# Optimization experiments

Measured on AMD Instinct MI355X. Metric: run time of the kernel, lower is better.

## Reference

```python
import jax, jax.numpy as jnp
import numpy as np

B, L = 16384, 200
N_USERS, N_ITEMS, N_CATS, N_DUR = 1_000_000, 100_000, 1000, 50
UD, ID, CD, DD, SD = 64, 64, 16, 8, 64
UDENSE, IDENSE = 25, 3
CONCAT = UD + ID + CD + DD + UDENSE + IDENSE + SD  # 244
NE, EH, EO, NT = 8, 256, 128, 2
T1, T2 = 64, 32  # tower dims
AH1, AH2 = 64, 16  # DIN attention hidden dims
NEG_INF = -1e9


def setup_inputs() -> dict:
    key = jax.random.key(0)
    ks = iter(jax.random.split(key, 40))
    nrm = lambda shape, s: jax.random.normal(next(ks), shape, jnp.float32) * s
    inp = {
        'user_id': jax.random.randint(next(ks), (B,), 0, N_USERS),
        'item_id': jax.random.randint(next(ks), (B,), 0, N_ITEMS),
        'item_category': jax.random.randint(next(ks), (B,), 0, N_CATS),
        'item_dur_bkt': jax.random.randint(next(ks), (B,), 0, N_DUR),
        'user_dense': jax.random.normal(next(ks), (B, UDENSE), jnp.float32),
        'item_dense': jax.random.normal(next(ks), (B, IDENSE), jnp.float32),
        'history_seq': jax.random.randint(next(ks), (B, L), 0, N_ITEMS + 1),
    }
    # embeddings (std=0.01 as in _init_weights); hist row 0 is padding_idx -> zero
    inp['user_E'] = nrm((N_USERS, UD), 0.01)
    inp['item_E'] = nrm((N_ITEMS, ID), 0.01)
    inp['cat_E'] = nrm((N_CATS, CD), 0.01)
    inp['dur_E'] = nrm((N_DUR, DD), 0.01)
    inp['hist_E'] = nrm((N_ITEMS + 1, SD), 0.01).at[0].set(0.0)
    inp['Wproj'] = nrm((ID, SD), 0.12)  # xavier-ish for target_proj (no bias)
    # DIN attention MLP: 4*SD -> 64 -> 16 -> 1
    inp['aW1'] = nrm((4 * SD, AH1), 0.06); inp['ab1'] = jnp.zeros((AH1,), jnp.float32)
    inp['aW2'] = nrm((AH1, AH2), 0.15);    inp['ab2'] = jnp.zeros((AH2,), jnp.float32)
    inp['aW3'] = nrm((AH2, 1), 0.3);       inp['ab3'] = jnp.zeros((1,), jnp.float32)
    # stacked experts: concat -> 256 -> 128 (ReLU both)
    inp['eW1'] = nrm((NE, CONCAT, EH), 0.06); inp['eb1'] = jnp.zeros((NE, EH), jnp.float32)
    inp['eW2'] = nrm((NE, EH, EO), 0.06);     inp['eb2'] = jnp.zeros((NE, EO), jnp.float32)
    # per-task gates: concat -> NE softmax
    inp['gW'] = nrm((NT, CONCAT, NE), 0.06); inp['gb'] = jnp.zeros((NT, NE), jnp.float32)
    # stacked towers: 128 -> 64 -> 32 -> 1
    inp['tW1'] = nrm((NT, EO, T1), 0.09); inp['tb1'] = jnp.zeros((NT, T1), jnp.float32)
    inp['tW2'] = nrm((NT, T1, T2), 0.12); inp['tb2'] = jnp.zeros((NT, T2), jnp.float32)
    inp['tW3'] = nrm((NT, T2, 1), 0.17);  inp['tb3'] = jnp.zeros((NT, 1), jnp.float32)
    return inp


def reference(user_id, item_id, item_category, item_dur_bkt, user_dense, item_dense,
              history_seq, user_E, item_E, cat_E, dur_E, hist_E, Wproj,
              aW1, ab1, aW2, ab2, aW3, ab3,
              eW1, eb1, eW2, eb2, gW, gb,
              tW1, tb1, tW2, tb2, tW3, tb3):
    # --- feature encoding ---
    i_emb = item_E[item_id]            # (B, ID)
    u_emb = user_E[user_id]            # (B, UD)
    c_emb = cat_E[item_category]       # (B, CD)
    d_emb = dur_E[item_dur_bkt]        # (B, DD)
    h_emb = hist_E[history_seq]        # (B, L, SD)
    tgt = (i_emb @ Wproj)[:, None, :]  # (B, 1, SD)
    t = jnp.broadcast_to(tgt, h_emb.shape)
    # DIN attention features: [target, hist, target-hist, target*hist]
    feat = jnp.concatenate([t, h_emb, t - h_emb, t * h_emb], axis=-1)  # (B, L, 4*SD)
    h = jax.nn.relu(feat @ aW1 + ab1)
    h = jax.nn.relu(h @ aW2 + ab2)
    scores = (h @ aW3 + ab3)[..., 0]   # (B, L)
    scores = jnp.where(history_seq == 0, NEG_INF, scores)
    attn = jax.nn.softmax(scores, axis=-1)
    pooled = jnp.einsum('bl,bld->bd', attn, h_emb)  # (B, SD)
    shared = jnp.concatenate([u_emb, i_emb, c_emb, d_emb, user_dense, item_dense, pooled], axis=-1)  # (B, CONCAT)
    # --- experts (batched GEMM) ---
    eh = jax.nn.relu(jnp.einsum('bc,ech->beh', shared, eW1) + eb1)
    eo = jax.nn.relu(jnp.einsum('beh,eho->beo', eh, eW2) + eb2)  # (B, NE, EO)
    # --- per-task gating + towers ---
    gate = jax.nn.softmax(jnp.einsum('bc,tce->bte', shared, gW) + gb, axis=-1)  # (B, T, NE)
    ti = jnp.einsum('bte,beo->bto', gate, eo)  # (B, T, EO)
    x = jax.nn.relu(jnp.einsum('bto,toh->bth', ti, tW1) + tb1)
    x = jax.nn.relu(jnp.einsum('bth,thk->btk', x, tW2) + tb2)
    logit = (jnp.einsum('btk,tkj->btj', x, tW3) + tb3)[..., 0]  # (B, T)
    pred = jax.nn.sigmoid(logit)
    return pred[:, 0], pred[:, 1]
```

## Files before the change

kernel.cpp:

```cpp
#include <hip/hip_runtime.h>
#include <hip/hip_bf16.h>
#include <cstdint>
#include <cmath>


typedef __attribute__((ext_vector_type(8))) short bfrag;
typedef __attribute__((ext_vector_type(4))) float f32x4;

__device__ __forceinline__ unsigned short f2bf(float f) {
  __hip_bfloat16 h = __float2bfloat16(f);
  return __builtin_bit_cast(unsigned short, h);
}
__device__ __forceinline__ float bf2f(unsigned short b) {
  union { unsigned u; float f; } v; v.u = ((unsigned)b) << 16;
  return v.f;
}
__device__ __forceinline__ float bfLo(unsigned hv) {
  union { unsigned u; float f; } v; v.u = hv << 16;
  return v.f;
}
__device__ __forceinline__ float bfHi(unsigned hv) {
  union { unsigned u; float f; } v; v.u = hv & 0xffff0000u;
  return v.f;
}

#define SWZ(row, col) ((col) ^ (((row) & 7) << 3))

static constexpr size_t WS_ATTNB = 0;
static constexpr size_t WS_AW2T  = WS_ATTNB + 16384;
static constexpr size_t WS_A13   = WS_AW2T + 2048;
static constexpr size_t WS_EW1T  = WS_A13 + 16384;
static constexpr size_t WS_EW2T  = WS_EW1T + 1048576;
static constexpr size_t WS_HISTB = WS_EW2T + 524288;
static constexpr size_t WS_TGT   = WS_HISTB + 12800256;
static constexpr size_t WS_TA    = WS_TGT + 2097152;
static constexpr size_t WS_SHP   = WS_TA + 4194304;
static constexpr size_t WS_EO    = WS_SHP + 8388608;
static constexpr size_t WS_GWB   = WS_EO + 33554432;
static constexpr size_t WS_TW1B  = WS_GWB + 8192;
static constexpr size_t WS_TW2B  = WS_TW1B + 32768;

__launch_bounds__(256)
__global__ void k0_prep(const float* __restrict__ aW1, const float* __restrict__ aW2,
                        const float* __restrict__ eW1, const float* __restrict__ eW2,
                        const float* __restrict__ hist_E,
                        const float* __restrict__ gW, const float* __restrict__ tW1,
                        const float* __restrict__ tW2,
                        unsigned short* __restrict__ attnBt, unsigned short* __restrict__ aW2t,
                        float* __restrict__ A13,
                        unsigned short* __restrict__ eW1t, unsigned short* __restrict__ eW2t,
                        unsigned short* __restrict__ hist_b,
                        unsigned short* __restrict__ gWb, unsigned short* __restrict__ tW1b,
                        unsigned short* __restrict__ tW2b) {
  int tid = blockIdx.x * blockDim.x + threadIdx.x;
  int nth = gridDim.x * blockDim.x;
  for (int i = tid; i < 64 * 128; i += nth) {
    int n = i >> 7, k = i & 127;
    float v = (k < 64) ? (aW1[(64 + k) * 64 + n] - aW1[(128 + k) * 64 + n])
                       : aW1[(128 + k) * 64 + n];
    attnBt[i] = f2bf(v);
  }
  for (int i = tid; i < 64 * 64; i += nth) {
    int k = i >> 6, n = i & 63;
    A13[i] = aW1[k * 64 + n] + aW1[(128 + k) * 64 + n];
  }
  for (int i = tid; i < 16 * 64; i += nth) {
    int n = i >> 6, k = i & 63;
    aW2t[i] = f2bf(aW2[k * 16 + n]);
  }
  for (int i = tid; i < 8 * 256 * 256; i += nth) {
    int e = i >> 16, n = (i >> 8) & 255, k = i & 255;
    eW1t[i] = (k < 244) ? f2bf(eW1[(e * 244 + k) * 256 + n]) : (unsigned short)0;
  }
  for (int i = tid; i < 8 * 128 * 256; i += nth) {
    int e = i >> 15, n = (i >> 8) & 127, k = i & 255;
    eW2t[i] = f2bf(eW2[(e * 256 + k) * 128 + n]);
  }
  for (int i = tid; i < 16 * 256; i += nth) {
    int n = i >> 8, k = i & 255, t = n >> 3, e = n & 7;
    gWb[i] = (k < 244) ? f2bf(gW[(t * 244 + k) * 8 + e]) : (unsigned short)0;
  }
  for (int i = tid; i < 2 * 64 * 128; i += nth) {
    int t = i >> 13, n = (i >> 7) & 63, k = i & 127;
    tW1b[i] = f2bf(tW1[(t * 128 + k) * 64 + n]);
  }
  for (int i = tid; i < 2 * 32 * 64; i += nth) {
    int t = i >> 11, n = (i >> 6) & 31, k = i & 63;
    tW2b[i] = f2bf(tW2[(t * 64 + k) * 32 + n]);
  }
  for (int i = tid; i < 100001 * 64; i += nth) hist_b[i] = f2bf(hist_E[i]);
}

__launch_bounds__(256)
__global__ void k1_tgt(const int* __restrict__ item_id, const float* __restrict__ item_E,
                       const float* __restrict__ Wproj, const float* __restrict__ A13,
                       const float* __restrict__ ab1,
                       unsigned short* __restrict__ tgt, float* __restrict__ tA) {
  __shared__ float Wp[64 * 64], A13s[64 * 64], ab1s[64];
  __shared__ float ivb[4][64], tbuf[4][64];
  int tid = threadIdx.x, w = tid >> 6, lane = tid & 63;
  for (int i = tid; i < 4096; i += 256) { Wp[i] = Wproj[i]; A13s[i] = A13[i]; }
  if (tid < 64) ab1s[tid] = ab1[tid];
  __syncthreads();
  int b0 = blockIdx.x * 16;
  for (int it = 0; it < 4; ++it) {
    int b = b0 + w * 4 + it;
    int iid = item_id[b];
    ivb[w][lane] = item_E[(size_t)iid * 64 + lane];
    __syncthreads();
    float t = 0.f;
#pragma unroll 8
    for (int k = 0; k < 64; ++k) t += ivb[w][k] * Wp[k * 64 + lane];
    tbuf[w][lane] = t;
    __syncthreads();
    float ta = ab1s[lane];
#pragma unroll 8
    for (int k = 0; k < 64; ++k) ta += tbuf[w][k] * A13s[k * 64 + lane];
    tgt[(size_t)b * 64 + lane] = f2bf(t);
    tA[(size_t)b * 64 + lane] = ta;
  }
}

__launch_bounds__(256)
__global__ void k3a_assemble(const int* __restrict__ user_id, const int* __restrict__ item_id,
                             const int* __restrict__ item_cat, const int* __restrict__ item_dur,
                             const float* __restrict__ user_dense, const float* __restrict__ item_dense,
                             const float* __restrict__ user_E, const float* __restrict__ item_E,
                             const float* __restrict__ cat_E, const float* __restrict__ dur_E,
                             unsigned short* __restrict__ shared_p) {
  int tid = threadIdx.x, w = tid >> 6, lane = tid & 63;
  int b = blockIdx.x * 4 + w;
  unsigned short* row = shared_p + (size_t)b * 256;
  row[lane]      = f2bf(user_E[(size_t)user_id[b] * 64 + lane]);
  row[64 + lane] = f2bf(item_E[(size_t)item_id[b] * 64 + lane]);
  if (lane < 16) row[128 + lane] = f2bf(cat_E[item_cat[b] * 16 + lane]);
  if (lane < 8)  row[144 + lane] = f2bf(dur_E[item_dur[b] * 8 + lane]);
  if (lane < 25) row[152 + lane] = f2bf(user_dense[b * 25 + lane]);
  if (lane < 3)  row[177 + lane] = f2bf(item_dense[b * 3 + lane]);
  if (lane < 12) row[244 + lane] = 0;
}

__launch_bounds__(256, 5)
__global__ void k2_attn(const int* __restrict__ hist_seq, const unsigned short* __restrict__ hist_b,
                        const unsigned short* __restrict__ tgt, const float* __restrict__ tA,
                        const unsigned short* __restrict__ attnBt_g, const unsigned short* __restrict__ aW2t_g,
                        const float* __restrict__ ab2, const float* __restrict__ aW3,
                        unsigned short* __restrict__ shared_p) {
  __shared__ unsigned short sH1[208 * 64];
  __shared__ int   ids[208];
  __shared__ float tv[64], tAv[64];
  __shared__ float sSc[208];
  __shared__ float red[8];
  __shared__ float pbuf[512];
  int b = blockIdx.x;
  int tid = threadIdx.x, w = tid >> 6, lane = tid & 63;
  int lr = lane & 15, g = lane >> 4;

  if (tid < 208) ids[tid] = (tid < 200) ? hist_seq[(size_t)b * 200 + tid] : 0;
  if (tid < 64) tv[tid] = bf2f(tgt[(size_t)b * 64 + tid]);
  else if (tid < 128) tAv[tid - 64] = tA[(size_t)b * 64 + (tid - 64)];

  bfrag b2fr[2];
#pragma unroll
  for (int kk = 0; kk < 2; ++kk)
    b2fr[kk] = *(const bfrag*)(aW2t_g + lr * 64 + kk * 32 + g * 8);
  float ab2v = ab2[lr];
  float aW3v = aW3[lr];
  __syncthreads();

  {
    int n = tid >> 2, k0 = (tid & 3) * 16;
    const unsigned short* rowp = attnBt_g + n * 128;
    unsigned short a23[16], a4[16], mo[16];
    *(uint4*)(a23)     = *(const uint4*)(rowp + k0);
    *(uint4*)(a23 + 8) = *(const uint4*)(rowp + k0 + 8);
    *(uint4*)(a4)      = *(const uint4*)(rowp + 64 + k0);
    *(uint4*)(a4 + 8)  = *(const uint4*)(rowp + 64 + k0 + 8);
#pragma unroll
    for (int i = 0; i < 16; ++i)
      mo[i] = f2bf(bf2f(a23[i]) + tv[k0 + i] * bf2f(a4[i]));
    *(uint4*)(sH1 + n * 64 + SWZ(n, k0))     = *(uint4*)(mo);
    *(uint4*)(sH1 + n * 64 + SWZ(n, k0 + 8)) = *(uint4*)(mo + 8);
  }
  __syncthreads();
  bfrag bfr[4][2];
#pragma unroll
  for (int nt = 0; nt < 4; ++nt)
#pragma unroll
    for (int kk = 0; kk < 2; ++kk) {
      int n = nt * 16 + lr;
      bfr[nt][kk] = *(const bfrag*)(sH1 + n * 64 + SWZ(n, kk * 32 + g * 8));
    }
  __syncthreads();

  for (int mt = w; mt < 13; mt += 4) {
    int m = mt * 16 + lr;
    const unsigned short* hrow = hist_b + (size_t)ids[m] * 64;
    bfrag h0 = *(const bfrag*)(hrow + g * 8);
    bfrag h1 = *(const bfrag*)(hrow + 32 + g * 8);
    f32x4 acc[4] = {{0.f,0.f,0.f,0.f},{0.f,0.f,0.f,0.f},{0.f,0.f,0.f,0.f},{0.f,0.f,0.f,0.f}};
#pragma unroll
    for (int nt = 0; nt < 4; ++nt) {
      acc[nt] = __builtin_amdgcn_mfma_f32_16x16x32_bf16(h0, bfr[nt][0], acc[nt], 0, 0, 0);
      acc[nt] = __builtin_amdgcn_mfma_f32_16x16x32_bf16(h1, bfr[nt][1], acc[nt], 0, 0, 0);
    }
#pragma unroll
    for (int nt = 0; nt < 4; ++nt) {
      int n = nt * 16 + lr;
      float ta = tAv[n];
#pragma unroll
      for (int r = 0; r < 4; ++r) {
        float v = fmaxf(acc[nt][r] + ta, 0.f);
        int mm = mt * 16 + g * 4 + r;
        sH1[mm * 64 + SWZ(mm, n)] = f2bf(v);
      }
    }
  }
  __syncthreads();

  for (int mt = w; mt < 13; mt += 4) {
    f32x4 acc = {0.f, 0.f, 0.f, 0.f};
    int m = mt * 16 + lr;
#pragma unroll
    for (int kk = 0; kk < 2; ++kk) {
      int k0 = kk * 32 + g * 8;
      bfrag a = *(const bfrag*)(sH1 + m * 64 + SWZ(m, k0));
      acc = __builtin_amdgcn_mfma_f32_16x16x32_bf16(a, b2fr[kk], acc, 0, 0, 0);
    }
    float sc[4];
#pragma unroll
    for (int r = 0; r < 4; ++r) sc[r] = fmaxf(acc[r] + ab2v, 0.f) * aW3v;
#pragma unroll
    for (int d = 1; d < 16; d <<= 1)
#pragma unroll
      for (int r = 0; r < 4; ++r) sc[r] += __shfl_xor(sc[r], d);
    if (lr == 0) {
      int mr = mt * 16 + g * 4;
      sSc[mr] = sc[0]; sSc[mr + 1] = sc[1]; sSc[mr + 2] = sc[2]; sSc[mr + 3] = sc[3];
    }
  }
  __syncthreads();

  bool valid = false; float sc0 = 0.f;
  if (tid < 200 && ids[tid] != 0) { valid = true; sc0 = sSc[tid]; }
  float v = valid ? sc0 : -3.0e38f;
#pragma unroll
  for (int d = 1; d < 64; d <<= 1) v = fmaxf(v, __shfl_xor(v, d));
  if (lane == 0) red[w] = v;
  __syncthreads();
  float mx = fmaxf(fmaxf(red[0], red[1]), fmaxf(red[2], red[3]));
  float p = valid ? __expf(sc0 - mx) : 0.f;
  float s = p;
#pragma unroll
  for (int d = 1; d < 64; d <<= 1) s += __shfl_xor(s, d);
  if (lane == 0) red[4 + w] = s;
  if (tid < 208) sSc[tid] = p;
  __syncthreads();
  float denom = red[4] + red[5] + red[6] + red[7] + 1e-30f;

  {
    int hp = lane >> 5, hl = lane & 31;
    float a0 = 0.f, a1 = 0.f;
    for (int i = 0; i < 25; ++i) {
      int l = w * 50 + hp * 25 + i;
      unsigned hv = *(const unsigned*)(hist_b + (size_t)ids[l] * 64 + 2 * hl);
      float pw = sSc[l];
      a0 += pw * bfLo(hv);
      a1 += pw * bfHi(hv);
    }
    pbuf[(w * 2 + hp) * 64 + 2 * hl]     = a0;
    pbuf[(w * 2 + hp) * 64 + 2 * hl + 1] = a1;
  }
  __syncthreads();
  if (tid < 64) {
    float tot = 0.f;
#pragma unroll
    for (int c = 0; c < 8; ++c) tot += pbuf[c * 64 + tid];
    shared_p[(size_t)b * 256 + 180 + tid] = f2bf(tot / denom);
  }
}

__launch_bounds__(256, 2)
__global__ void k3b_experts(const unsigned short* __restrict__ shared_p,
                            const unsigned short* __restrict__ eW1t, const unsigned short* __restrict__ eW2t,
                            const float* __restrict__ eb1, const float* __restrict__ eb2,
                            unsigned short* __restrict__ eo_ws) {
  __shared__ unsigned short sX[64 * 256];
  __shared__ unsigned short sW[256 * 64];
  int tid = threadIdx.x, w = tid >> 6, lane = tid & 63;
  int e = blockIdx.x & 7;
  int b0 = (blockIdx.x >> 3) * 64;
  int lr = lane & 15, g = lane >> 4;

  for (int j = tid; j < 2048; j += 256) {
    int r = j >> 5, ke = (j & 31) * 8;
    uint4 v = *(const uint4*)(shared_p + (size_t)(b0 + r) * 256 + ke);
    *(uint4*)(sX + r * 256 + SWZ(r, ke)) = v;
  }
  f32x4 acc[16];
#pragma unroll
  for (int i = 0; i < 16; ++i) acc[i] = (f32x4){0.f, 0.f, 0.f, 0.f};
  const unsigned short* w1 = eW1t + (size_t)e * 256 * 256;
  for (int c = 0; c < 4; ++c) {
    __syncthreads();
    for (int j = tid; j < 2048; j += 256) {
      int n = j >> 3, ke = (j & 7) * 8;
      uint4 v = *(const uint4*)(w1 + n * 256 + c * 64 + ke);
      *(uint4*)(sW + n * 64 + SWZ(n, ke)) = v;
    }
    __syncthreads();
    int m = w * 16 + lr;
#pragma unroll
    for (int kk = 0; kk < 2; ++kk) {
      int kabs = c * 64 + kk * 32 + g * 8;
      bfrag a = *(const bfrag*)(sX + m * 256 + SWZ(m, kabs));
      int kloc = kk * 32 + g * 8;
#pragma unroll
      for (int nt = 0; nt < 16; ++nt) {
        int n = nt * 16 + lr;
        bfrag bb = *(const bfrag*)(sW + n * 64 + SWZ(n, kloc));
        acc[nt] = __builtin_amdgcn_mfma_f32_16x16x32_bf16(a, bb, acc[nt], 0, 0, 0);
      }
    }
  }
  __syncthreads();
#pragma unroll
  for (int nt = 0; nt < 16; ++nt) {
    int n = nt * 16 + lr;
    float bb = eb1[e * 256 + n];
#pragma unroll
    for (int r = 0; r < 4; ++r) {
      float vv = fmaxf(acc[nt][r] + bb, 0.f);
      int mm = w * 16 + g * 4 + r;
      sX[mm * 256 + SWZ(mm, n)] = f2bf(vv);
    }
  }
  f32x4 acc2[8];
#pragma unroll
  for (int i = 0; i < 8; ++i) acc2[i] = (f32x4){0.f, 0.f, 0.f, 0.f};
  const unsigned short* w2 = eW2t + (size_t)e * 128 * 256;
  for (int c = 0; c < 4; ++c) {
    __syncthreads();
    for (int j = tid; j < 1024; j += 256) {
      int n = j >> 3, ke = (j & 7) * 8;
      uint4 v = *(const uint4*)(w2 + n * 256 + c * 64 + ke);
      *(uint4*)(sW + n * 64 + SWZ(n, ke)) = v;
    }
    __syncthreads();
    int m = w * 16 + lr;
#pragma unroll
    for (int kk = 0; kk < 2; ++kk) {
      int kabs = c * 64 + kk * 32 + g * 8;
      bfrag a = *(const bfrag*)(sX + m * 256 + SWZ(m, kabs));
      int kloc = kk * 32 + g * 8;
#pragma unroll
      for (int nt = 0; nt < 8; ++nt) {
        int n = nt * 16 + lr;
        bfrag bb = *(const bfrag*)(sW + n * 64 + SWZ(n, kloc));
        acc2[nt] = __builtin_amdgcn_mfma_f32_16x16x32_bf16(a, bb, acc2[nt], 0, 0, 0);
      }
    }
  }
#pragma unroll
  for (int nt = 0; nt < 8; ++nt) {
    int n = nt * 16 + lr;
    float bb = eb2[e * 128 + n];
#pragma unroll
    for (int r = 0; r < 4; ++r) {
      float vv = fmaxf(acc2[nt][r] + bb, 0.f);
      int mm = w * 16 + g * 4 + r;
      eo_ws[((size_t)(b0 + mm) * 8 + e) * 128 + n] = f2bf(vv);
    }
  }
}

__launch_bounds__(256, 3)
__global__ void k4_tail(const unsigned short* __restrict__ shared_p, const unsigned short* __restrict__ eo_ws,
                        const unsigned short* __restrict__ gWb, const float* __restrict__ gb,
                        const unsigned short* __restrict__ tW1b, const float* __restrict__ tb1,
                        const unsigned short* __restrict__ tW2b, const float* __restrict__ tb2,
                        const float* __restrict__ tW3, const float* __restrict__ tb3,
                        float* __restrict__ out) {
  __shared__ float sGL[32 * 17];
  __shared__ unsigned short sTi[2 * 32 * 128];
  __shared__ unsigned short sX1[2 * 32 * 64];
  int tid = threadIdx.x, w = tid >> 6, lane = tid & 63;
  int lr = lane & 15, g = lane >> 4;
  int b0 = blockIdx.x * 32;

  if (w < 2) {
    int m = b0 + w * 16 + lr;
    f32x4 acc = {0.f, 0.f, 0.f, 0.f};
#pragma unroll
    for (int kk = 0; kk < 8; ++kk) {
      bfrag a = *(const bfrag*)(shared_p + (size_t)m * 256 + kk * 32 + g * 8);
      bfrag bb = *(const bfrag*)(gWb + lr * 256 + kk * 32 + g * 8);
      acc = __builtin_amdgcn_mfma_f32_16x16x32_bf16(a, bb, acc, 0, 0, 0);
    }
    float gbv = gb[lr];
#pragma unroll
    for (int r = 0; r < 4; ++r)
      sGL[(w * 16 + g * 4 + r) * 17 + lr] = acc[r] + gbv;
  }
  __syncthreads();

  if (tid < 64) {
    int row = tid >> 1, t = tid & 1;
    float* p = sGL + row * 17 + t * 8;
    float mx = -3e38f;
#pragma unroll
    for (int e = 0; e < 8; ++e) mx = fmaxf(mx, p[e]);
    float sum = 0.f; float pe[8];
#pragma unroll
    for (int e = 0; e < 8; ++e) { pe[e] = __expf(p[e] - mx); sum += pe[e]; }
    float inv = 1.f / sum;
#pragma unroll
    for (int e = 0; e < 8; ++e) p[e] = pe[e] * inv;
  }
  __syncthreads();

  {
    int row = tid >> 3, q = tid & 7, t = q >> 2, o0 = (q & 3) * 32;
    const float* gp = sGL + row * 17 + t * 8;
    float accL[16], accH[16];
#pragma unroll
    for (int j = 0; j < 16; ++j) { accL[j] = 0.f; accH[j] = 0.f; }
    const unsigned short* base = eo_ws + ((size_t)(b0 + row) * 8) * 128 + o0;
#pragma unroll
    for (int e = 0; e < 8; ++e) {
      float ge = gp[e];
      const unsigned short* p = base + e * 128;
#pragma unroll
      for (int c = 0; c < 4; ++c) {
        uint4 v = *(const uint4*)(p + c * 8);
        const unsigned* u = (const unsigned*)&v;
#pragma unroll
        for (int j = 0; j < 4; ++j) {
          accL[c * 4 + j] += ge * bfLo(u[j]);
          accH[c * 4 + j] += ge * bfHi(u[j]);
        }
      }
    }
    unsigned short ob[32];
#pragma unroll
    for (int j = 0; j < 16; ++j) {
      ob[2 * j]     = f2bf(accL[j]);
      ob[2 * j + 1] = f2bf(accH[j]);
    }
#pragma unroll
    for (int c = 0; c < 4; ++c)
      *(uint4*)(sTi + t * 4096 + row * 128 + SWZ(row, o0 + c * 8)) = *(const uint4*)(ob + c * 8);
  }
  __syncthreads();

  int t = w >> 1, mt = w & 1;
  {
    f32x4 acc[4] = {{0.f,0.f,0.f,0.f},{0.f,0.f,0.f,0.f},{0.f,0.f,0.f,0.f},{0.f,0.f,0.f,0.f}};
    int ml = mt * 16 + lr;
#pragma unroll
    for (int kk = 0; kk < 4; ++kk) {
      bfrag a = *(const bfrag*)(sTi + t * 4096 + ml * 128 + SWZ(ml, kk * 32 + g * 8));
#pragma unroll
      for (int nt = 0; nt < 4; ++nt) {
        bfrag bb = *(const bfrag*)(tW1b + t * 8192 + (nt * 16 + lr) * 128 + kk * 32 + g * 8);
        acc[nt] = __builtin_amdgcn_mfma_f32_16x16x32_bf16(a, bb, acc[nt], 0, 0, 0);
      }
    }
#pragma unroll
    for (int nt = 0; nt < 4; ++nt) {
      int n = nt * 16 + lr;
      float bias = tb1[t * 64 + n];
#pragma unroll
      for (int r = 0; r < 4; ++r) {
        float x = fmaxf(acc[nt][r] + bias, 0.f);
        int row = mt * 16 + g * 4 + r;
        sX1[t * 2048 + row * 64 + SWZ(row, n)] = f2bf(x);
      }
    }
  }
  __syncthreads();

  {
    f32x4 acc[2] = {{0.f,0.f,0.f,0.f},{0.f,0.f,0.f,0.f}};
    int ml = mt * 16 + lr;
#pragma unroll
    for (int kk = 0; kk < 2; ++kk) {
      bfrag a = *(const bfrag*)(sX1 + t * 2048 + ml * 64 + SWZ(ml, kk * 32 + g * 8));
#pragma unroll
      for (int nt = 0; nt < 2; ++nt) {
        bfrag bb = *(const bfrag*)(tW2b + t * 2048 + (nt * 16 + lr) * 64 + kk * 32 + g * 8);
        acc[nt] = __builtin_amdgcn_mfma_f32_16x16x32_bf16(a, bb, acc[nt], 0, 0, 0);
      }
    }
    float part[4] = {0.f, 0.f, 0.f, 0.f};
#pragma unroll
    for (int nt = 0; nt < 2; ++nt) {
      int n = nt * 16 + lr;
      float bias = tb2[t * 32 + n];
      float w3 = tW3[t * 32 + n];
#pragma unroll
      for (int r = 0; r < 4; ++r)
        part[r] += fmaxf(acc[nt][r] + bias, 0.f) * w3;
    }
#pragma unroll
    for (int d = 1; d < 16; d <<= 1)
#pragma unroll
      for (int r = 0; r < 4; ++r) part[r] += __shfl_xor(part[r], d);
    if (lr == 0) {
      float b3 = tb3[t];
#pragma unroll
      for (int r = 0; r < 4; ++r) {
        float logit = part[r] + b3;
        out[(size_t)t * 16384 + b0 + mt * 16 + g * 4 + r] = 1.f / (1.f + __expf(-logit));
      }
    }
  }
}

extern "C" void kernel_launch(void* const* d_in, const int* in_sizes, int n_in,
                              void* d_out, int out_size, void* d_ws, size_t ws_size,
                              hipStream_t stream) {
  const int*   user_id    = (const int*)  d_in[0];
  const int*   item_id    = (const int*)  d_in[1];
  const int*   item_cat   = (const int*)  d_in[2];
  const int*   item_dur   = (const int*)  d_in[3];
  const float* user_dense = (const float*)d_in[4];
  const float* item_dense = (const float*)d_in[5];
  const int*   hist_seq   = (const int*)  d_in[6];
  const float* user_E     = (const float*)d_in[7];
  const float* item_E     = (const float*)d_in[8];
  const float* cat_E      = (const float*)d_in[9];
  const float* dur_E      = (const float*)d_in[10];
  const float* hist_E     = (const float*)d_in[11];
  const float* Wproj      = (const float*)d_in[12];
  const float* aW1        = (const float*)d_in[13];
  const float* ab1        = (const float*)d_in[14];
  const float* aW2        = (const float*)d_in[15];
  const float* ab2        = (const float*)d_in[16];
  const float* aW3        = (const float*)d_in[17];
  const float* eW1        = (const float*)d_in[19];
  const float* eb1        = (const float*)d_in[20];
  const float* eW2        = (const float*)d_in[21];
  const float* eb2        = (const float*)d_in[22];
  const float* gW         = (const float*)d_in[23];
  const float* gb         = (const float*)d_in[24];
  const float* tW1        = (const float*)d_in[25];
  const float* tb1        = (const float*)d_in[26];
  const float* tW2        = (const float*)d_in[27];
  const float* tb2        = (const float*)d_in[28];
  const float* tW3        = (const float*)d_in[29];
  const float* tb3        = (const float*)d_in[30];
  float* out = (float*)d_out;
  char* ws = (char*)d_ws;

  unsigned short* attnBt  = (unsigned short*)(ws + WS_ATTNB);
  unsigned short* aW2t    = (unsigned short*)(ws + WS_AW2T);
  float*          A13     = (float*)         (ws + WS_A13);
  unsigned short* eW1t    = (unsigned short*)(ws + WS_EW1T);
  unsigned short* eW2t    = (unsigned short*)(ws + WS_EW2T);
  unsigned short* hist_b  = (unsigned short*)(ws + WS_HISTB);
  unsigned short* tgt     = (unsigned short*)(ws + WS_TGT);
  float*          tA      = (float*)         (ws + WS_TA);
  unsigned short* shared_p= (unsigned short*)(ws + WS_SHP);
  unsigned short* eo_ws   = (unsigned short*)(ws + WS_EO);
  unsigned short* gWb     = (unsigned short*)(ws + WS_GWB);
  unsigned short* tW1b    = (unsigned short*)(ws + WS_TW1B);
  unsigned short* tW2b    = (unsigned short*)(ws + WS_TW2B);

  k0_prep<<<2048, 256, 0, stream>>>(aW1, aW2, eW1, eW2, hist_E, gW, tW1, tW2,
                                    attnBt, aW2t, A13, eW1t, eW2t, hist_b,
                                    gWb, tW1b, tW2b);
  k1_tgt<<<1024, 256, 0, stream>>>(item_id, item_E, Wproj, A13, ab1, tgt, tA);
  k3a_assemble<<<4096, 256, 0, stream>>>(user_id, item_id, item_cat, item_dur,
                                         user_dense, item_dense, user_E, item_E,
                                         cat_E, dur_E, shared_p);
  k2_attn<<<16384, 256, 0, stream>>>(hist_seq, hist_b, tgt, tA, attnBt, aW2t,
                                     ab2, aW3, shared_p);
  k3b_experts<<<2048, 256, 0, stream>>>(shared_p, eW1t, eW2t, eb1, eb2, eo_ws);
  k4_tail<<<512, 256, 0, stream>>>(shared_p, eo_ws, gWb, gb, tW1b, tb1, tW2b, tb2,
                                   tW3, tb3, out);
}
```

Measured before the change: 257.9 us.

## Fuse assembly into attention, MFMA target projection, per-wave attention pipeline

Folds the shared-feature assembly kernel into the attention kernel, removing one launch. The target projection kernel now uses bf16 MFMA with a precomposed Wproj·A13 matrix built in prep. The attention kernel keeps each wave's layer-1 output in a private LDS buffer and runs layer 2 right away, which drops one block-wide barrier and shrinks LDS so occupancy can rise to 6. Precomposing the weights and rounding to bf16 changes numerics slightly.

```diff
diff --git a/kernel.cpp b/kernel.cpp
--- a/kernel.cpp
+++ b/kernel.cpp
@@ -39,19 +39,21 @@
 static constexpr size_t WS_GWB   = WS_EO + 33554432;
 static constexpr size_t WS_TW1B  = WS_GWB + 8192;
 static constexpr size_t WS_TW2B  = WS_TW1B + 32768;
+static constexpr size_t WS_WPB   = WS_TW2B + 8192;
+static constexpr size_t WS_WAB   = WS_WPB + 8192;
 
 __launch_bounds__(256)
 __global__ void k0_prep(const float* __restrict__ aW1, const float* __restrict__ aW2,
                         const float* __restrict__ eW1, const float* __restrict__ eW2,
                         const float* __restrict__ hist_E,
                         const float* __restrict__ gW, const float* __restrict__ tW1,
-                        const float* __restrict__ tW2,
+                        const float* __restrict__ tW2, const float* __restrict__ Wproj,
                         unsigned short* __restrict__ attnBt, unsigned short* __restrict__ aW2t,
-                        float* __restrict__ A13,
                         unsigned short* __restrict__ eW1t, unsigned short* __restrict__ eW2t,
                         unsigned short* __restrict__ hist_b,
                         unsigned short* __restrict__ gWb, unsigned short* __restrict__ tW1b,
-                        unsigned short* __restrict__ tW2b) {
+                        unsigned short* __restrict__ tW2b,
+                        unsigned short* __restrict__ Wpb, unsigned short* __restrict__ WAb) {
   int tid = blockIdx.x * blockDim.x + threadIdx.x;
   int nth = gridDim.x * blockDim.x;
   for (int i = tid; i < 64 * 128; i += nth) {
@@ -60,14 +62,21 @@
                        : aW1[(128 + k) * 64 + n];
     attnBt[i] = f2bf(v);
   }
-  for (int i = tid; i < 64 * 64; i += nth) {
-    int k = i >> 6, n = i & 63;
-    A13[i] = aW1[k * 64 + n] + aW1[(128 + k) * 64 + n];
-  }
   for (int i = tid; i < 16 * 64; i += nth) {
     int n = i >> 6, k = i & 63;
     aW2t[i] = f2bf(aW2[k * 16 + n]);
   }
+  for (int i = tid; i < 64 * 64; i += nth) {
+    int n = i >> 6, k = i & 63;
+    Wpb[i] = f2bf(Wproj[k * 64 + n]);
+  }
+  for (int i = tid; i < 64 * 64; i += nth) {
+    int n = i >> 6, k = i & 63;
+    float s = 0.f;
+    for (int j = 0; j < 64; ++j)
+      s += Wproj[k * 64 + j] * (aW1[j * 64 + n] + aW1[(128 + j) * 64 + n]);
+    WAb[i] = f2bf(s);
+  }
   for (int i = tid; i < 8 * 256 * 256; i += nth) {
     int e = i >> 16, n = (i >> 8) & 255, k = i & 255;
     eW1t[i] = (k < 244) ? f2bf(eW1[(e * 244 + k) * 256 + n]) : (unsigned short)0;
@@ -93,60 +102,64 @@
 
 __launch_bounds__(256)
 __global__ void k1_tgt(const int* __restrict__ item_id, const float* __restrict__ item_E,
-                       const float* __restrict__ Wproj, const float* __restrict__ A13,
+                       const unsigned short* __restrict__ Wpb, const unsigned short* __restrict__ WAb,
                        const float* __restrict__ ab1,
                        unsigned short* __restrict__ tgt, float* __restrict__ tA) {
-  __shared__ float Wp[64 * 64], A13s[64 * 64], ab1s[64];
-  __shared__ float ivb[4][64], tbuf[4][64];
   int tid = threadIdx.x, w = tid >> 6, lane = tid & 63;
-  for (int i = tid; i < 4096; i += 256) { Wp[i] = Wproj[i]; A13s[i] = A13[i]; }
-  if (tid < 64) ab1s[tid] = ab1[tid];
-  __syncthreads();
-  int b0 = blockIdx.x * 16;
-  for (int it = 0; it < 4; ++it) {
-    int b = b0 + w * 4 + it;
-    int iid = item_id[b];
-    ivb[w][lane] = item_E[(size_t)iid * 64 + lane];
-    __syncthreads();
-    float t = 0.f;
-#pragma unroll 8
-    for (int k = 0; k < 64; ++k) t += ivb[w][k] * Wp[k * 64 + lane];
-    tbuf[w][lane] = t;
-    __syncthreads();
-    float ta = ab1s[lane];
-#pragma unroll 8
-    for (int k = 0; k < 64; ++k) ta += tbuf[w][k] * A13s[k * 64 + lane];
-    tgt[(size_t)b * 64 + lane] = f2bf(t);
-    tA[(size_t)b * 64 + lane] = ta;
-  }
-}
-
-__launch_bounds__(256)
-__global__ void k3a_assemble(const int* __restrict__ user_id, const int* __restrict__ item_id,
-                             const int* __restrict__ item_cat, const int* __restrict__ item_dur,
-                             const float* __restrict__ user_dense, const float* __restrict__ item_dense,
-                             const float* __restrict__ user_E, const float* __restrict__ item_E,
-                             const float* __restrict__ cat_E, const float* __restrict__ dur_E,
-                             unsigned short* __restrict__ shared_p) {
-  int tid = threadIdx.x, w = tid >> 6, lane = tid & 63;
-  int b = blockIdx.x * 4 + w;
-  unsigned short* row = shared_p + (size_t)b * 256;
-  row[lane]      = f2bf(user_E[(size_t)user_id[b] * 64 + lane]);
-  row[64 + lane] = f2bf(item_E[(size_t)item_id[b] * 64 + lane]);
-  if (lane < 16) row[128 + lane] = f2bf(cat_E[item_cat[b] * 16 + lane]);
-  if (lane < 8)  row[144 + lane] = f2bf(dur_E[item_dur[b] * 8 + lane]);
-  if (lane < 25) row[152 + lane] = f2bf(user_dense[b * 25 + lane]);
-  if (lane < 3)  row[177 + lane] = f2bf(item_dense[b * 3 + lane]);
-  if (lane < 12) row[244 + lane] = 0;
-}
-
-__launch_bounds__(256, 5)
+  int lr = lane & 15, g = lane >> 4;
+  int b0 = blockIdx.x * 64 + w * 16;
+  int iid = item_id[b0 + lr];
+  bfrag ia[2];
+#pragma unroll
+  for (int kk = 0; kk < 2; ++kk) {
+    const float* src = item_E + (size_t)iid * 64 + kk * 32 + g * 8;
+    float4 x = *(const float4*)src;
+    float4 y = *(const float4*)(src + 4);
+    bfrag r;
+    r[0] = (short)f2bf(x.x); r[1] = (short)f2bf(x.y);
+    r[2] = (short)f2bf(x.z); r[3] = (short)f2bf(x.w);
+    r[4] = (short)f2bf(y.x); r[5] = (short)f2bf(y.y);
+    r[6] = (short)f2bf(y.z); r[7] = (short)f2bf(y.w);
+    ia[kk] = r;
+  }
+  f32x4 at[4], aa[4];
+#pragma unroll
+  for (int i = 0; i < 4; ++i) { at[i] = (f32x4){0,0,0,0}; aa[i] = (f32x4){0,0,0,0}; }
+#pragma unroll
+  for (int kk = 0; kk < 2; ++kk)
+#pragma unroll
+    for (int nt = 0; nt < 4; ++nt) {
+      bfrag wp = *(const bfrag*)(Wpb + (nt * 16 + lr) * 64 + kk * 32 + g * 8);
+      at[nt] = __builtin_amdgcn_mfma_f32_16x16x32_bf16(ia[kk], wp, at[nt], 0, 0, 0);
+      bfrag wa = *(const bfrag*)(WAb + (nt * 16 + lr) * 64 + kk * 32 + g * 8);
+      aa[nt] = __builtin_amdgcn_mfma_f32_16x16x32_bf16(ia[kk], wa, aa[nt], 0, 0, 0);
+    }
+#pragma unroll
+  for (int nt = 0; nt < 4; ++nt) {
+    int n = nt * 16 + lr;
+    float b1 = ab1[n];
+#pragma unroll
+    for (int r = 0; r < 4; ++r) {
+      int m = b0 + g * 4 + r;
+      tgt[(size_t)m * 64 + n] = f2bf(at[nt][r]);
+      tA[(size_t)m * 64 + n] = aa[nt][r] + b1;
+    }
+  }
+}
+
+__launch_bounds__(256, 6)
 __global__ void k2_attn(const int* __restrict__ hist_seq, const unsigned short* __restrict__ hist_b,
                         const unsigned short* __restrict__ tgt, const float* __restrict__ tA,
                         const unsigned short* __restrict__ attnBt_g, const unsigned short* __restrict__ aW2t_g,
                         const float* __restrict__ ab2, const float* __restrict__ aW3,
+                        const int* __restrict__ user_id, const int* __restrict__ item_id,
+                        const int* __restrict__ item_cat, const int* __restrict__ item_dur,
+                        const float* __restrict__ user_dense, const float* __restrict__ item_dense,
+                        const float* __restrict__ user_E, const float* __restrict__ item_E,
+                        const float* __restrict__ cat_E, const float* __restrict__ dur_E,
                         unsigned short* __restrict__ shared_p) {
-  __shared__ unsigned short sH1[208 * 64];
+  __shared__ unsigned short sM[64 * 64];
+  __shared__ unsigned short wbuf[4][16 * 64];
   __shared__ int   ids[208];
   __shared__ float tv[64], tAv[64];
   __shared__ float sSc[208];
@@ -160,12 +173,23 @@
   if (tid < 64) tv[tid] = bf2f(tgt[(size_t)b * 64 + tid]);
   else if (tid < 128) tAv[tid - 64] = tA[(size_t)b * 64 + (tid - 64)];
 
+  {
+    unsigned short* row = shared_p + (size_t)b * 256;
+    if (tid < 64)       row[tid] = f2bf(user_E[(size_t)user_id[b] * 64 + tid]);
+    else if (tid < 128) row[tid] = f2bf(item_E[(size_t)item_id[b] * 64 + (tid - 64)]);
+    else if (tid < 144) row[tid] = f2bf(cat_E[item_cat[b] * 16 + (tid - 128)]);
+    else if (tid < 152) row[tid] = f2bf(dur_E[item_dur[b] * 8 + (tid - 144)]);
+    else if (tid < 177) row[tid] = f2bf(user_dense[b * 25 + (tid - 152)]);
+    else if (tid < 180) row[tid] = f2bf(item_dense[b * 3 + (tid - 177)]);
+    else if (tid >= 244) row[tid] = 0;
+  }
+
   bfrag b2fr[2];
 #pragma unroll
   for (int kk = 0; kk < 2; ++kk)
     b2fr[kk] = *(const bfrag*)(aW2t_g + lr * 64 + kk * 32 + g * 8);
-  float ab2v = ab2[lr];
-  float aW3v = aW3[lr];
+  f32x4 ab2v4 = *(const f32x4*)(ab2 + g * 4);
+  f32x4 aW3v4 = *(const f32x4*)(aW3 + g * 4);
   __syncthreads();
 
   {
@@ -179,65 +203,48 @@
 #pragma unroll
     for (int i = 0; i < 16; ++i)
       mo[i] = f2bf(bf2f(a23[i]) + tv[k0 + i] * bf2f(a4[i]));
-    *(uint4*)(sH1 + n * 64 + SWZ(n, k0))     = *(uint4*)(mo);
-    *(uint4*)(sH1 + n * 64 + SWZ(n, k0 + 8)) = *(uint4*)(mo + 8);
-  }
-  __syncthreads();
-  bfrag bfr[4][2];
-#pragma unroll
-  for (int nt = 0; nt < 4; ++nt)
-#pragma unroll
-    for (int kk = 0; kk < 2; ++kk) {
-      int n = nt * 16 + lr;
-      bfr[nt][kk] = *(const bfrag*)(sH1 + n * 64 + SWZ(n, kk * 32 + g * 8));
-    }
-  __syncthreads();
-
+    *(uint4*)(sM + n * 64 + SWZ(n, k0))     = *(uint4*)(mo);
+    *(uint4*)(sM + n * 64 + SWZ(n, k0 + 8)) = *(uint4*)(mo + 8);
+  }
+  __syncthreads();
+
+  unsigned short* wb = wbuf[w];
   for (int mt = w; mt < 13; mt += 4) {
     int m = mt * 16 + lr;
     const unsigned short* hrow = hist_b + (size_t)ids[m] * 64;
     bfrag h0 = *(const bfrag*)(hrow + g * 8);
     bfrag h1 = *(const bfrag*)(hrow + 32 + g * 8);
-    f32x4 acc[4] = {{0.f,0.f,0.f,0.f},{0.f,0.f,0.f,0.f},{0.f,0.f,0.f,0.f},{0.f,0.f,0.f,0.f}};
+    f32x4 acc[4] = {{0,0,0,0},{0,0,0,0},{0,0,0,0},{0,0,0,0}};
 #pragma unroll
     for (int nt = 0; nt < 4; ++nt) {
-      acc[nt] = __builtin_amdgcn_mfma_f32_16x16x32_bf16(h0, bfr[nt][0], acc[nt], 0, 0, 0);
-      acc[nt] = __builtin_amdgcn_mfma_f32_16x16x32_bf16(h1, bfr[nt][1], acc[nt], 0, 0, 0);
+      bfrag m0f = *(const bfrag*)(sM + (nt * 16 + lr) * 64 + SWZ(nt * 16 + lr, g * 8));
+      acc[nt] = __builtin_amdgcn_mfma_f32_16x16x32_bf16(m0f, h0, acc[nt], 0, 0, 0);
+      bfrag m1f = *(const bfrag*)(sM + (nt * 16 + lr) * 64 + SWZ(nt * 16 + lr, 32 + g * 8));
+      acc[nt] = __builtin_amdgcn_mfma_f32_16x16x32_bf16(m1f, h1, acc[nt], 0, 0, 0);
     }
 #pragma unroll
     for (int nt = 0; nt < 4; ++nt) {
-      int n = nt * 16 + lr;
-      float ta = tAv[n];
-#pragma unroll
-      for (int r = 0; r < 4; ++r) {
-        float v = fmaxf(acc[nt][r] + ta, 0.f);
-        int mm = mt * 16 + g * 4 + r;
-        sH1[mm * 64 + SWZ(mm, n)] = f2bf(v);
-      }
-    }
-  }
-  __syncthreads();
-
-  for (int mt = w; mt < 13; mt += 4) {
-    f32x4 acc = {0.f, 0.f, 0.f, 0.f};
-    int m = mt * 16 + lr;
+      f32x4 ta4 = *(const f32x4*)(tAv + nt * 16 + g * 4);
+      unsigned lo = (unsigned)f2bf(fmaxf(acc[nt][0] + ta4[0], 0.f))
+                  | ((unsigned)f2bf(fmaxf(acc[nt][1] + ta4[1], 0.f)) << 16);
+      unsigned hi = (unsigned)f2bf(fmaxf(acc[nt][2] + ta4[2], 0.f))
+                  | ((unsigned)f2bf(fmaxf(acc[nt][3] + ta4[3], 0.f)) << 16);
+      uint2 pk; pk.x = lo; pk.y = hi;
+      *(uint2*)(wb + lr * 64 + SWZ(lr, nt * 16 + g * 4)) = pk;
+    }
+    f32x4 acc2 = {0.f, 0.f, 0.f, 0.f};
 #pragma unroll
     for (int kk = 0; kk < 2; ++kk) {
-      int k0 = kk * 32 + g * 8;
-      bfrag a = *(const bfrag*)(sH1 + m * 64 + SWZ(m, k0));
-      acc = __builtin_amdgcn_mfma_f32_16x16x32_bf16(a, b2fr[kk], acc, 0, 0, 0);
-    }
-    float sc[4];
-#pragma unroll
-    for (int r = 0; r < 4; ++r) sc[r] = fmaxf(acc[r] + ab2v, 0.f) * aW3v;
-#pragma unroll
-    for (int d = 1; d < 16; d <<= 1)
-#pragma unroll
-      for (int r = 0; r < 4; ++r) sc[r] += __shfl_xor(sc[r], d);
-    if (lr == 0) {
-      int mr = mt * 16 + g * 4;
-      sSc[mr] = sc[0]; sSc[mr + 1] = sc[1]; sSc[mr + 2] = sc[2]; sSc[mr + 3] = sc[3];
-    }
+      bfrag hb = *(const bfrag*)(wb + lr * 64 + SWZ(lr, kk * 32 + g * 8));
+      acc2 = __builtin_amdgcn_mfma_f32_16x16x32_bf16(b2fr[kk], hb, acc2, 0, 0, 0);
+    }
+    float p = 0.f;
+#pragma unroll
+    for (int r = 0; r < 4; ++r)
+      p += fmaxf(acc2[r] + ab2v4[r], 0.f) * aW3v4[r];
+    p += __shfl_xor(p, 16);
+    p += __shfl_xor(p, 32);
+    if (lane < 16) sSc[m] = p;
   }
   __syncthreads();
 
@@ -555,7 +562,6 @@
 
   unsigned short* attnBt  = (unsigned short*)(ws + WS_ATTNB);
   unsigned short* aW2t    = (unsigned short*)(ws + WS_AW2T);
-  float*          A13     = (float*)         (ws + WS_A13);
   unsigned short* eW1t    = (unsigned short*)(ws + WS_EW1T);
   unsigned short* eW2t    = (unsigned short*)(ws + WS_EW2T);
   unsigned short* hist_b  = (unsigned short*)(ws + WS_HISTB);
@@ -566,16 +572,18 @@
   unsigned short* gWb     = (unsigned short*)(ws + WS_GWB);
   unsigned short* tW1b    = (unsigned short*)(ws + WS_TW1B);
   unsigned short* tW2b    = (unsigned short*)(ws + WS_TW2B);
-
-  k0_prep<<<2048, 256, 0, stream>>>(aW1, aW2, eW1, eW2, hist_E, gW, tW1, tW2,
-                                    attnBt, aW2t, A13, eW1t, eW2t, hist_b,
-                                    gWb, tW1b, tW2b);
-  k1_tgt<<<1024, 256, 0, stream>>>(item_id, item_E, Wproj, A13, ab1, tgt, tA);
-  k3a_assemble<<<4096, 256, 0, stream>>>(user_id, item_id, item_cat, item_dur,
-                                         user_dense, item_dense, user_E, item_E,
-                                         cat_E, dur_E, shared_p);
+  unsigned short* Wpb     = (unsigned short*)(ws + WS_WPB);
+  unsigned short* WAb     = (unsigned short*)(ws + WS_WAB);
+
+  k0_prep<<<2048, 256, 0, stream>>>(aW1, aW2, eW1, eW2, hist_E, gW, tW1, tW2, Wproj,
+                                    attnBt, aW2t, eW1t, eW2t, hist_b,
+                                    gWb, tW1b, tW2b, Wpb, WAb);
+  k1_tgt<<<256, 256, 0, stream>>>(item_id, item_E, Wpb, WAb, ab1, tgt, tA);
   k2_attn<<<16384, 256, 0, stream>>>(hist_seq, hist_b, tgt, tA, attnBt, aW2t,
-                                     ab2, aW3, shared_p);
+                                     ab2, aW3,
+                                     user_id, item_id, item_cat, item_dur,
+                                     user_dense, item_dense, user_E, item_E,
+                                     cat_E, dur_E, shared_p);
   k3b_experts<<<2048, 256, 0, stream>>>(shared_p, eW1t, eW2t, eb1, eb2, eo_ws);
   k4_tail<<<512, 256, 0, stream>>>(shared_p, eo_ws, gWb, gb, tW1b, tb1, tW2b, tb2,
                                    tW3, tb3, out);
```

Measured after the change: 381.5 us. 47.9% more time.
